# Kernel optimization log

Measured on AMD Instinct MI355X. Metric: run time of the kernel, lower is better.

Reference implementation:

```python
import jax, jax.numpy as jnp
import numpy as np

N_SUBWORDS = 8192
N_WORDS = 6000
HIDDEN = 1024


def setup_inputs() -> dict:
    key = jax.random.key(0)
    k_h, k_s, k_w = jax.random.split(key, 3)
    hidden_states = jax.random.normal(k_h, (N_SUBWORDS, HIDDEN), dtype=jnp.float32)
    # sorted start indices of words; ends are inclusive and contiguous up to the next start
    word_starts = jnp.sort(jax.random.randint(k_s, (N_WORDS,), 0, N_SUBWORDS, dtype=jnp.int64))
    nxt = jnp.concatenate([word_starts[1:], jnp.array([N_SUBWORDS], dtype=jnp.int64)])
    word_ends = jnp.maximum(nxt - 1, word_starts)  # inclusive ends, >= starts
    # params of self.subword_attn = Linear(hidden_size, 1)
    w_attn = jax.random.normal(k_w, (HIDDEN, 1), dtype=jnp.float32) * 0.02
    b_attn = jnp.zeros((1,), dtype=jnp.float32)
    return {
        "hidden_states": hidden_states,
        "word_starts": word_starts,
        "word_ends": word_ends,
        "w_attn": w_attn,
        "b_attn": b_attn,
    }


def reference(hidden_states, word_starts, word_ends, w_attn, b_attn):
    """Word-encoder masked attention pooling (wl-coref _wordencoder_attn_scores + pooling).

    hidden_states: [n_subwords, hidden]
    word_starts/word_ends: [n_words] inclusive span boundaries over subwords
    Returns pooled word embeddings: [n_words, hidden]
    """
    n_sub = hidden_states.shape[0]
    pos = jnp.arange(n_sub)  # [n_subwords]
    # torch: (arange >= starts) * (arange < ends+1)  -> inclusive end mask
    mask = (pos[None, :] >= word_starts[:, None]) & (pos[None, :] <= word_ends[:, None])
    # per-subword scalar score: Linear(hidden, 1), broadcast to [n_words, n_subwords]
    scores = (hidden_states @ w_attn + b_attn).T  # [1, n_subwords]
    # torch adds log(mask.float()) == -inf outside span; scores are finite
    logits = jnp.where(mask, scores, -jnp.inf)
    attn = jax.nn.softmax(logits, axis=1)  # [n_words, n_subwords]
    # pool subword embeddings into word embeddings
    return attn @ hidden_states  # [n_words, hidden]
```

## Files before the change

### kernel.cpp

```cpp
#include <hip/hip_runtime.h>
#include <hip/hip_bf16.h>
#include <math.h>

#define N_SUBWORDS 8192
#define N_WORDS    6000
#define HIDDEN     1024

__global__ __launch_bounds__(256) void coref_scores_kernel(
    const float* __restrict__ hs,
    const float* __restrict__ w_attn,
    const float* __restrict__ b_attn,
    float* __restrict__ scores)
{
    const int gtid = blockIdx.x * blockDim.x + threadIdx.x;
    const int row  = gtid >> 6;
    const int lane = threadIdx.x & 63;
    if (row >= N_SUBWORDS) return;

    const float4* __restrict__ hrow = (const float4*)(hs + (size_t)row * HIDDEN);
    const float4* __restrict__ wv   = (const float4*)w_attn;

    float sum = 0.f;
#pragma unroll
    for (int i = 0; i < 4; ++i) {
        const int idx = lane + 64 * i;
        float4 h  = hrow[idx];
        float4 ww = wv[idx];
        sum += h.x * ww.x + h.y * ww.y + h.z * ww.z + h.w * ww.w;
    }
#pragma unroll
    for (int off = 32; off > 0; off >>= 1)
        sum += __shfl_down(sum, off, 64);

    if (lane == 0)
        scores[row] = sum + b_attn[0];
}

__global__ __launch_bounds__(256) void coref_pool_kernel(
    const float* __restrict__ hs,
    const int*   __restrict__ starts,
    const int*   __restrict__ ends,
    const float* __restrict__ scores,
    float*       __restrict__ out)
{
    const int w = blockIdx.x;
    if (w >= N_WORDS) return;

    const int s0 = starts[w];
    const int s1 = ends[w];

    float m = -INFINITY;
    for (int s = s0; s <= s1; ++s)
        m = fmaxf(m, scores[s]);
    float l = 0.f;
    for (int s = s0; s <= s1; ++s)
        l += expf(scores[s] - m);
    const float inv_l = 1.f / l;

    const int d = threadIdx.x * 4;
    float4 acc = make_float4(0.f, 0.f, 0.f, 0.f);
    for (int s = s0; s <= s1; ++s) {
        const float wt = expf(scores[s] - m) * inv_l;
        float4 h = *(const float4*)(hs + (size_t)s * HIDDEN + d);
        acc.x += wt * h.x;
        acc.y += wt * h.y;
        acc.z += wt * h.z;
        acc.w += wt * h.w;
    }
    *(float4*)(out + (size_t)w * HIDDEN + d) = acc;
}

extern "C" void kernel_launch(void* const* d_in, const int* in_sizes, int n_in,
                              void* d_out, int out_size, void* d_ws, size_t ws_size,
                              hipStream_t stream) {
    const float* hs      = (const float*)d_in[0];
    const int*   starts  = (const int*)d_in[1];
    const int*   ends    = (const int*)d_in[2];
    const float* w_attn  = (const float*)d_in[3];
    const float* b_attn  = (const float*)d_in[4];
    float*       out     = (float*)d_out;
    float*       scores  = (float*)d_ws;

    coref_scores_kernel<<<dim3((N_SUBWORDS * 64) / 256), dim3(256), 0, stream>>>(
        hs, w_attn, b_attn, scores);

    coref_pool_kernel<<<dim3(N_WORDS), dim3(256), 0, stream>>>(
        hs, starts, ends, scores, out);
}
```

Baseline: 96.65 us.

## Fuse score computation into pooling kernel with online softmax

Removes the separate scores kernel. Each word block now computes subword scores on the fly with a block-wide dot-product reduction, then folds them into an online-softmax accumulator during the single pooling pass. This saves a kernel launch, the scores round trip, and the two serial max and sum passes over scores. In exchange each subword row's dot product is recomputed by every word that covers it, and each loop iteration adds a __syncthreads.

```diff
diff --git a/kernel.cpp b/kernel.cpp
--- a/kernel.cpp
+++ b/kernel.cpp
@@ -6,84 +6,80 @@
 #define N_WORDS    6000
 #define HIDDEN     1024
 
-__global__ __launch_bounds__(256) void coref_scores_kernel(
-    const float* __restrict__ hs,
-    const float* __restrict__ w_attn,
-    const float* __restrict__ b_attn,
-    float* __restrict__ scores)
-{
-    const int gtid = blockIdx.x * blockDim.x + threadIdx.x;
-    const int row  = gtid >> 6;
-    const int lane = threadIdx.x & 63;
-    if (row >= N_SUBWORDS) return;
-
-    const float4* __restrict__ hrow = (const float4*)(hs + (size_t)row * HIDDEN);
-    const float4* __restrict__ wv   = (const float4*)w_attn;
-
-    float sum = 0.f;
-#pragma unroll
-    for (int i = 0; i < 4; ++i) {
-        const int idx = lane + 64 * i;
-        float4 h  = hrow[idx];
-        float4 ww = wv[idx];
-        sum += h.x * ww.x + h.y * ww.y + h.z * ww.z + h.w * ww.w;
-    }
-#pragma unroll
-    for (int off = 32; off > 0; off >>= 1)
-        sum += __shfl_down(sum, off, 64);
-
-    if (lane == 0)
-        scores[row] = sum + b_attn[0];
-}
-
-__global__ __launch_bounds__(256) void coref_pool_kernel(
+__global__ __launch_bounds__(256) void coref_fused_kernel(
     const float* __restrict__ hs,
     const int*   __restrict__ starts,
     const int*   __restrict__ ends,
-    const float* __restrict__ scores,
+    const float* __restrict__ w_attn,
+    const float* __restrict__ b_attn,
     float*       __restrict__ out)
 {
-    const int w = blockIdx.x;
-    if (w >= N_WORDS) return;
+    __shared__ float red[8];
+
+    const int w    = blockIdx.x;
+    const int tid  = threadIdx.x;
+    const int lane = tid & 63;
+    const int wid  = tid >> 6;
 
     const int s0 = starts[w];
     const int s1 = ends[w];
 
-    float m = -INFINITY;
-    for (int s = s0; s <= s1; ++s)
-        m = fmaxf(m, scores[s]);
-    float l = 0.f;
-    for (int s = s0; s <= s1; ++s)
-        l += expf(scores[s] - m);
+    const float4 wv = ((const float4*)w_attn)[tid];
+    const float  b  = b_attn[0];
+
+    float  m = 0.f, l = 1.f;
+    float4 acc = make_float4(0.f, 0.f, 0.f, 0.f);
+
+    for (int s = s0; s <= s1; ++s) {
+        float4 h = ((const float4*)(hs + (size_t)s * HIDDEN))[tid];
+
+        float part = h.x * wv.x + h.y * wv.y + h.z * wv.z + h.w * wv.w;
+        #pragma unroll
+        for (int off = 32; off > 0; off >>= 1)
+            part += __shfl_down(part, off, 64);
+
+        const int slot = ((s - s0) & 1) << 2;
+        if (lane == 0) red[slot + wid] = part;
+        __syncthreads();
+        const float score =
+            red[slot + 0] + red[slot + 1] + red[slot + 2] + red[slot + 3] + b;
+
+        if (s == s0) {
+            m = score;
+            l = 1.f;
+            acc = h;
+        } else {
+            const float mn    = fmaxf(m, score);
+            const float alpha = __expf(m - mn);
+            const float p     = __expf(score - mn);
+            m = mn;
+            l = l * alpha + p;
+            acc.x = acc.x * alpha + p * h.x;
+            acc.y = acc.y * alpha + p * h.y;
+            acc.z = acc.z * alpha + p * h.z;
+            acc.w = acc.w * alpha + p * h.w;
+        }
+    }
+
     const float inv_l = 1.f / l;
-
-    const int d = threadIdx.x * 4;
-    float4 acc = make_float4(0.f, 0.f, 0.f, 0.f);
-    for (int s = s0; s <= s1; ++s) {
-        const float wt = expf(scores[s] - m) * inv_l;
-        float4 h = *(const float4*)(hs + (size_t)s * HIDDEN + d);
-        acc.x += wt * h.x;
-        acc.y += wt * h.y;
-        acc.z += wt * h.z;
-        acc.w += wt * h.w;
-    }
-    *(float4*)(out + (size_t)w * HIDDEN + d) = acc;
+    float4 o;
+    o.x = acc.x * inv_l;
+    o.y = acc.y * inv_l;
+    o.z = acc.z * inv_l;
+    o.w = acc.w * inv_l;
+    ((float4*)(out + (size_t)w * HIDDEN))[tid] = o;
 }
 
 extern "C" void kernel_launch(void* const* d_in, const int* in_sizes, int n_in,
                               void* d_out, int out_size, void* d_ws, size_t ws_size,
                               hipStream_t stream) {
-    const float* hs      = (const float*)d_in[0];
-    const int*   starts  = (const int*)d_in[1];
-    const int*   ends    = (const int*)d_in[2];
-    const float* w_attn  = (const float*)d_in[3];
-    const float* b_attn  = (const float*)d_in[4];
-    float*       out     = (float*)d_out;
-    float*       scores  = (float*)d_ws;
+    const float* hs     = (const float*)d_in[0];
+    const int*   starts = (const int*)d_in[1];
+    const int*   ends   = (const int*)d_in[2];
+    const float* w_attn = (const float*)d_in[3];
+    const float* b_attn = (const float*)d_in[4];
+    float*       out    = (float*)d_out;
 
-    coref_scores_kernel<<<dim3((N_SUBWORDS * 64) / 256), dim3(256), 0, stream>>>(
-        hs, w_attn, b_attn, scores);
-
-    coref_pool_kernel<<<dim3(N_WORDS), dim3(256), 0, stream>>>(
-        hs, starts, ends, scores, out);
+    coref_fused_kernel<<<dim3(N_WORDS), dim3(256), 0, stream>>>(
+        hs, starts, ends, w_attn, b_attn, out);
 }
```

Result: faster. 92.66 us (-4.1%).
